# Performance work log

Hardware: AMD Instinct MI355X
Metric: run time of the kernel (lower is better)

The kernel has to match this reference:

```python
import jax, jax.numpy as jnp
import numpy as np


def setup_inputs() -> dict:
    key = jax.random.key(0)
    ks = jax.random.split(key, 5)
    B, H, W, C = 64, 14, 14, 2048
    x = jax.random.normal(ks[0], (B, H, W, C), dtype=jnp.float32)
    # Glorot-ish scaled 1x1 conv weights (stored as [Cin, Cout])
    W1 = jax.random.normal(ks[1], (C, 64), dtype=jnp.float32) * (1.0 / np.sqrt(C))
    W2 = jax.random.normal(ks[2], (64, 16), dtype=jnp.float32) * (1.0 / np.sqrt(64))
    W3 = jax.random.normal(ks[3], (16, 8), dtype=jnp.float32) * (1.0 / np.sqrt(16))
    W4 = jax.random.normal(ks[4], (8, 1), dtype=jnp.float32) * (1.0 / np.sqrt(8))
    return {
        "x": x,
        "W1": W1, "b1": jnp.zeros((64,), jnp.float32),
        "W2": W2, "b2": jnp.zeros((16,), jnp.float32),
        "W3": W3, "b3": jnp.zeros((8,), jnp.float32),
        "W4": W4, "b4": jnp.zeros((1,), jnp.float32),
    }


def reference(x, W1, b1, W2, b2, W3, b3, W4, b4):
    # Dropout is identity at inference time.
    # 1x1 convs == per-pixel matmuls over channel dim.
    h = jax.nn.relu(jnp.einsum('bhwc,cd->bhwd', x, W1) + b1)   # [B,H,W,64]
    h = jax.nn.relu(jnp.einsum('bhwc,cd->bhwd', h, W2) + b2)   # [B,H,W,16]
    h = jax.nn.relu(jnp.einsum('bhwc,cd->bhwd', h, W3) + b3)   # [B,H,W,8]
    a = jax.nn.sigmoid(jnp.einsum('bhwc,cd->bhwd', h, W4) + b4)  # [B,H,W,1]
    # 'upsample' frozen ones-conv == broadcast of a over 2048 channels.
    gap_features = jnp.mean(a * x, axis=(1, 2))  # [B, 2048]
    gap_mask = jnp.mean(a, axis=(1, 2))          # [B, 1] (same value for all 2048 chans)
    return gap_features / gap_mask               # [B, 2048]
```

## Files before the change

### kernel.cpp

```cpp
#include <hip/hip_runtime.h>
#include <math.h>

#define NPIX 12544
#define CIN  2048
#define NB   64
#define PPIX 196

typedef short  bf16x8 __attribute__((ext_vector_type(8)));
typedef float  f32x4  __attribute__((ext_vector_type(4)));

__device__ inline unsigned short f2bf(float f) {
    unsigned int u = __float_as_uint(f);
    u = (u + 0x7fffu + ((u >> 16) & 1u)) >> 16;
    return (unsigned short)u;
}

__global__ __launch_bounds__(256) void conv_w1(
    const float* __restrict__ W1, unsigned short* __restrict__ W1t)
{
    const int id = blockIdx.x * 256 + threadIdx.x;
    const int n = id >> 11;
    const int k = id & 2047;
    W1t[id] = f2bf(W1[k * 64 + n]);
}

__global__ __launch_bounds__(64) void attn_scores_mfma(
    const float* __restrict__ x, const unsigned short* __restrict__ W1t,
    const float* __restrict__ b1,
    const float* __restrict__ W2, const float* __restrict__ b2,
    const float* __restrict__ W3, const float* __restrict__ b3,
    const float* __restrict__ W4, const float* __restrict__ b4,
    float* __restrict__ a_out)
{
    __shared__ float h1s[16][68];

    const int lane = threadIdx.x;
    const int l15  = lane & 15;
    const int q    = lane >> 4;
    const size_t pix0 = (size_t)blockIdx.x * 16;

    const float* xr = x + (pix0 + l15) * (size_t)CIN + q * 8;
    const unsigned short* wr = W1t + (size_t)l15 * CIN + q * 8;

    f32x4 acc[4] = {{0,0,0,0},{0,0,0,0},{0,0,0,0},{0,0,0,0}};

#pragma unroll 2
    for (int k0 = 0; k0 < CIN; k0 += 32) {
        float4 xa = *(const float4*)(xr + k0);
        float4 xb = *(const float4*)(xr + k0 + 4);
        bf16x8 af;
        af[0] = (short)f2bf(xa.x); af[1] = (short)f2bf(xa.y);
        af[2] = (short)f2bf(xa.z); af[3] = (short)f2bf(xa.w);
        af[4] = (short)f2bf(xb.x); af[5] = (short)f2bf(xb.y);
        af[6] = (short)f2bf(xb.z); af[7] = (short)f2bf(xb.w);
#pragma unroll
        for (int ct = 0; ct < 4; ++ct) {
            bf16x8 bfr = *(const bf16x8*)(wr + (size_t)ct * 16 * CIN + k0);
            acc[ct] = __builtin_amdgcn_mfma_f32_16x16x32_bf16(af, bfr, acc[ct], 0, 0, 0);
        }
    }

#pragma unroll
    for (int ct = 0; ct < 4; ++ct) {
        const float bias = b1[ct * 16 + l15];
#pragma unroll
        for (int r = 0; r < 4; ++r)
            h1s[q * 4 + r][ct * 16 + l15] = fmaxf(acc[ct][r] + bias, 0.f);
    }
    __syncthreads();

    if (lane < 16) {
        float hv[64];
#pragma unroll
        for (int i = 0; i < 16; ++i) {
            float4 t = *(const float4*)&h1s[lane][i * 4];
            hv[i*4+0] = t.x; hv[i*4+1] = t.y; hv[i*4+2] = t.z; hv[i*4+3] = t.w;
        }
        float h2[16];
#pragma unroll
        for (int j = 0; j < 16; ++j) {
            float s = b2[j];
#pragma unroll
            for (int k = 0; k < 64; ++k) s = fmaf(hv[k], W2[k * 16 + j], s);
            h2[j] = fmaxf(s, 0.f);
        }
        float h3[8];
#pragma unroll
        for (int j = 0; j < 8; ++j) {
            float s = b3[j];
#pragma unroll
            for (int k = 0; k < 16; ++k) s = fmaf(h2[k], W3[k * 8 + j], s);
            h3[j] = fmaxf(s, 0.f);
        }
        float z = b4[0];
#pragma unroll
        for (int k = 0; k < 8; ++k) z = fmaf(h3[k], W4[k], z);
        a_out[pix0 + lane] = 1.f / (1.f + expf(-z));
    }
}

__global__ __launch_bounds__(256) void gap_partial(
    const float* __restrict__ x, const float* __restrict__ a,
    float* __restrict__ part)
{
    const int b  = blockIdx.y;
    const int pz = blockIdx.z;
    const int c0 = (blockIdx.x * 256 + threadIdx.x) * 4;
    const float* xb = x + ((size_t)b * PPIX + pz * 98) * CIN + c0;
    const float* ab = a + b * PPIX + pz * 98;

    float4 s0 = {0,0,0,0}, s1 = {0,0,0,0};
#pragma unroll 4
    for (int p = 0; p < 98; p += 2) {
        const float a0 = ab[p], a1 = ab[p + 1];
        const float4 v0 = *(const float4*)(xb + (size_t)p * CIN);
        const float4 v1 = *(const float4*)(xb + (size_t)(p + 1) * CIN);
        s0.x = fmaf(a0, v0.x, s0.x); s0.y = fmaf(a0, v0.y, s0.y);
        s0.z = fmaf(a0, v0.z, s0.z); s0.w = fmaf(a0, v0.w, s0.w);
        s1.x = fmaf(a1, v1.x, s1.x); s1.y = fmaf(a1, v1.y, s1.y);
        s1.z = fmaf(a1, v1.z, s1.z); s1.w = fmaf(a1, v1.w, s1.w);
    }
    float4 r;
    r.x = s0.x + s1.x; r.y = s0.y + s1.y; r.z = s0.z + s1.z; r.w = s0.w + s1.w;
    *(float4*)(part + ((size_t)pz * NB + b) * CIN + c0) = r;
}

__global__ __launch_bounds__(512) void gap_final(
    const float* __restrict__ a, const float* __restrict__ part,
    float* __restrict__ out)
{
    __shared__ float red[512];
    const int b = blockIdx.x, t = threadIdx.x;
    red[t] = (t < PPIX) ? a[b * PPIX + t] : 0.f;
    __syncthreads();
#pragma unroll
    for (int s = 256; s > 0; s >>= 1) {
        if (t < s) red[t] += red[t + s];
        __syncthreads();
    }
    const float inv = 1.f / red[0];
    const int c0 = t * 4;
    const float4 p0 = *(const float4*)(part + ((size_t)0 * NB + b) * CIN + c0);
    const float4 p1 = *(const float4*)(part + ((size_t)1 * NB + b) * CIN + c0);
    float4 r;
    r.x = (p0.x + p1.x) * inv; r.y = (p0.y + p1.y) * inv;
    r.z = (p0.z + p1.z) * inv; r.w = (p0.w + p1.w) * inv;
    *(float4*)(out + (size_t)b * CIN + c0) = r;
}

extern "C" void kernel_launch(void* const* d_in, const int* in_sizes, int n_in,
                              void* d_out, int out_size, void* d_ws, size_t ws_size,
                              hipStream_t stream)
{
    const float* x  = (const float*)d_in[0];
    const float* W1 = (const float*)d_in[1];
    const float* b1 = (const float*)d_in[2];
    const float* W2 = (const float*)d_in[3];
    const float* b2 = (const float*)d_in[4];
    const float* W3 = (const float*)d_in[5];
    const float* b3 = (const float*)d_in[6];
    const float* W4 = (const float*)d_in[7];
    const float* b4 = (const float*)d_in[8];
    float* out = (float*)d_out;

    unsigned short* W1t = (unsigned short*)d_ws;
    float* a    = (float*)((char*)d_ws + (256 << 10));
    float* part = (float*)((char*)d_ws + (512 << 10));

    conv_w1<<<512, 256, 0, stream>>>(W1, W1t);
    attn_scores_mfma<<<NPIX / 16, 64, 0, stream>>>(x, W1t, b1, W2, b2, W3, b3, W4, b4, a);
    gap_partial<<<dim3(2, NB, 2), 256, 0, stream>>>(x, a, part);
    gap_final<<<NB, 512, 0, stream>>>(a, part, out);
}
```

Before: 197.4 us.

## Split K across 8 waves in attention MFMA and widen GAP pixel split

The attention-score kernel now uses 8 waves per 16-pixel block, each covering one eighth of the 2048 input channels. Partial accumulators are reduced through shared memory before bias and ReLU. The GAP partial kernel splits the 196 pixels into 7 chunks of 28 instead of 2 chunks of 98, which gives many more blocks, and the final kernel sums the 7 partials. Both changes aim at the low occupancy and long serial loops of the old launch shapes. The cost is extra shared-memory reduction, more syncs and more partial-sum traffic.

```diff
diff --git a/kernel.cpp b/kernel.cpp
--- a/kernel.cpp
+++ b/kernel.cpp
@@ -5,6 +5,8 @@
 #define CIN  2048
 #define NB   64
 #define PPIX 196
+#define NWV  8
+#define PCH  7
 
 typedef short  bf16x8 __attribute__((ext_vector_type(8)));
 typedef float  f32x4  __attribute__((ext_vector_type(4)));
@@ -24,7 +26,7 @@
     W1t[id] = f2bf(W1[k * 64 + n]);
 }
 
-__global__ __launch_bounds__(64) void attn_scores_mfma(
+__global__ __launch_bounds__(512) void attn_scores_mfma(
     const float* __restrict__ x, const unsigned short* __restrict__ W1t,
     const float* __restrict__ b1,
     const float* __restrict__ W2, const float* __restrict__ b2,
@@ -32,20 +34,24 @@
     const float* __restrict__ W4, const float* __restrict__ b4,
     float* __restrict__ a_out)
 {
+    __shared__ float part[NWV][16][68];
     __shared__ float h1s[16][68];
 
-    const int lane = threadIdx.x;
+    const int tid  = threadIdx.x;
+    const int lane = tid & 63;
+    const int wv   = tid >> 6;
     const int l15  = lane & 15;
     const int q    = lane >> 4;
     const size_t pix0 = (size_t)blockIdx.x * 16;
 
-    const float* xr = x + (pix0 + l15) * (size_t)CIN + q * 8;
-    const unsigned short* wr = W1t + (size_t)l15 * CIN + q * 8;
+    const int kb = wv * (CIN / NWV);
+    const float* xr = x + (pix0 + l15) * (size_t)CIN + kb + q * 8;
+    const unsigned short* wr = W1t + (size_t)l15 * CIN + kb + q * 8;
 
     f32x4 acc[4] = {{0,0,0,0},{0,0,0,0},{0,0,0,0},{0,0,0,0}};
 
-#pragma unroll 2
-    for (int k0 = 0; k0 < CIN; k0 += 32) {
+#pragma unroll
+    for (int k0 = 0; k0 < CIN / NWV; k0 += 32) {
         float4 xa = *(const float4*)(xr + k0);
         float4 xb = *(const float4*)(xr + k0 + 4);
         bf16x8 af;
@@ -61,19 +67,27 @@
     }
 
 #pragma unroll
-    for (int ct = 0; ct < 4; ++ct) {
-        const float bias = b1[ct * 16 + l15];
+    for (int ct = 0; ct < 4; ++ct)
 #pragma unroll
         for (int r = 0; r < 4; ++r)
-            h1s[q * 4 + r][ct * 16 + l15] = fmaxf(acc[ct][r] + bias, 0.f);
+            part[wv][q * 4 + r][ct * 16 + l15] = acc[ct][r];
+    __syncthreads();
+
+#pragma unroll
+    for (int e = tid; e < 16 * 64; e += 512) {
+        const int m = e >> 6, n = e & 63;
+        float v = b1[n];
+#pragma unroll
+        for (int w = 0; w < NWV; ++w) v += part[w][m][n];
+        h1s[m][n] = fmaxf(v, 0.f);
     }
     __syncthreads();
 
-    if (lane < 16) {
+    if (tid < 16) {
         float hv[64];
 #pragma unroll
         for (int i = 0; i < 16; ++i) {
-            float4 t = *(const float4*)&h1s[lane][i * 4];
+            float4 t = *(const float4*)&h1s[tid][i * 4];
             hv[i*4+0] = t.x; hv[i*4+1] = t.y; hv[i*4+2] = t.z; hv[i*4+3] = t.w;
         }
         float h2[16];
@@ -95,7 +109,7 @@
         float z = b4[0];
 #pragma unroll
         for (int k = 0; k < 8; ++k) z = fmaf(h3[k], W4[k], z);
-        a_out[pix0 + lane] = 1.f / (1.f + expf(-z));
+        a_out[pix0 + tid] = 1.f / (1.f + expf(-z));
     }
 }
 
@@ -105,13 +119,13 @@
 {
     const int b  = blockIdx.y;
     const int pz = blockIdx.z;
-    const int c0 = (blockIdx.x * 256 + threadIdx.x) * 4;
-    const float* xb = x + ((size_t)b * PPIX + pz * 98) * CIN + c0;
-    const float* ab = a + b * PPIX + pz * 98;
+    const int c0 = blockIdx.x * 1024 + threadIdx.x * 4;
+    const float* xb = x + ((size_t)b * PPIX + pz * 28) * CIN + c0;
+    const float* ab = a + b * PPIX + pz * 28;
 
     float4 s0 = {0,0,0,0}, s1 = {0,0,0,0};
 #pragma unroll 4
-    for (int p = 0; p < 98; p += 2) {
+    for (int p = 0; p < 28; p += 2) {
         const float a0 = ab[p], a1 = ab[p + 1];
         const float4 v0 = *(const float4*)(xb + (size_t)p * CIN);
         const float4 v1 = *(const float4*)(xb + (size_t)(p + 1) * CIN);
@@ -140,11 +154,13 @@
     }
     const float inv = 1.f / red[0];
     const int c0 = t * 4;
-    const float4 p0 = *(const float4*)(part + ((size_t)0 * NB + b) * CIN + c0);
-    const float4 p1 = *(const float4*)(part + ((size_t)1 * NB + b) * CIN + c0);
-    float4 r;
-    r.x = (p0.x + p1.x) * inv; r.y = (p0.y + p1.y) * inv;
-    r.z = (p0.z + p1.z) * inv; r.w = (p0.w + p1.w) * inv;
+    float4 r = {0,0,0,0};
+#pragma unroll
+    for (int pz = 0; pz < PCH; ++pz) {
+        const float4 p = *(const float4*)(part + ((size_t)pz * NB + b) * CIN + c0);
+        r.x += p.x; r.y += p.y; r.z += p.z; r.w += p.w;
+    }
+    r.x *= inv; r.y *= inv; r.z *= inv; r.w *= inv;
     *(float4*)(out + (size_t)b * CIN + c0) = r;
 }
 
@@ -168,7 +184,7 @@
     float* part = (float*)((char*)d_ws + (512 << 10));
 
     conv_w1<<<512, 256, 0, stream>>>(W1, W1t);
-    attn_scores_mfma<<<NPIX / 16, 64, 0, stream>>>(x, W1t, b1, W2, b2, W3, b3, W4, b4, a);
-    gap_partial<<<dim3(2, NB, 2), 256, 0, stream>>>(x, a, part);
+    attn_scores_mfma<<<NPIX / 16, 512, 0, stream>>>(x, W1t, b1, W2, b2, W3, b3, W4, b4, a);
+    gap_partial<<<dim3(2, NB, PCH), 256, 0, stream>>>(x, a, part);
     gap_final<<<NB, 512, 0, stream>>>(a, part, out);
 }
```

New measurement: 210.9 us. +6.8%, slower.
